# Kernel optimization log

Measured on AMD Instinct MI355X. Metric: run time of the kernel, lower is better.

The kernel has to match this reference:

```python
import jax, jax.numpy as jnp
import numpy as np

B, T, E, HD = 8, 2048, 1024, 64  # batch, seq (== n_ctx), n_embd, head_dim = n_embd // n_head


def setup_inputs() -> dict:
    key = jax.random.key(0)
    k1, k2, k3, k4 = jax.random.split(key, 4)
    x = jax.random.normal(k1, (B, T, E), dtype=jnp.float32)
    s = E ** -0.5  # Linear-like init scale
    Wq = jax.random.normal(k2, (E, HD), dtype=jnp.float32) * s
    Wk = jax.random.normal(k3, (E, HD), dtype=jnp.float32) * s
    Wv = jax.random.normal(k4, (E, HD), dtype=jnp.float32) * s
    return {"x": x, "Wq": Wq, "Wk": Wk, "Wv": Wv}


def reference(x, Wq, Wk, Wv):
    # q,k,v: [B, T, HD]
    q = jnp.einsum('bte,eh->bth', x, Wq)
    k = jnp.einsum('bte,eh->bth', x, Wk)
    v = jnp.einsum('bte,eh->bth', x, Wv)
    scale = k.shape[-1] ** -0.5
    # scores: [B, T, T]
    alpha = jnp.einsum('bqh,bkh->bqk', q, k) * scale
    causal = jnp.tril(jnp.ones((T, T), dtype=bool))
    alpha = jnp.where(causal, alpha, -jnp.inf)
    alpha = jax.nn.softmax(alpha, axis=-1)
    # dropout with p=0.0 is identity in eval
    h = jnp.einsum('bqk,bkh->bqh', alpha, v)  # [B, T, HD]
    return h
```

## Files before the change

### kernel.cpp

```cpp
#include <hip/hip_runtime.h>
#include <hip/hip_bf16.h>
#include <math.h>

#define BATCH 8
#define T 2048
#define E 1024
#define HD 64
#define BT (BATCH * T)

typedef __bf16 bf16_t;
typedef bf16_t bf16x4 __attribute__((ext_vector_type(4)));
typedef bf16_t bf16x8 __attribute__((ext_vector_type(8)));
typedef float f32x4 __attribute__((ext_vector_type(4)));

#define MFMA(a, b, c) __builtin_amdgcn_mfma_f32_16x16x32_bf16((a), (b), (c), 0, 0, 0)

#define QSCALE (0.125f * 1.44269504088896340736f)


__global__ __launch_bounds__(256) void prep_w(const float* __restrict__ Wq,
                                              const float* __restrict__ Wk,
                                              const float* __restrict__ Wv,
                                              bf16_t* __restrict__ WTt) {
    const int nt  = blockIdx.x >> 3;
    const int kc0 = (blockIdx.x & 7) * 128;
    const int tid = threadIdx.x;
    const int l16 = tid & 15;
    const int k8  = (kc0 >> 3) + (tid >> 4);
    const int n   = nt * 16 + l16;
    const int m   = n >> 6;
    const int col = n & 63;
    const float* W = (m == 0) ? Wq : (m == 1) ? Wk : Wv;
    const float scale = (m == 0) ? QSCALE : 1.0f;
    bf16x8 o;
#pragma unroll
    for (int j = 0; j < 8; j++) {
        o[j] = (bf16_t)(W[(size_t)(k8 * 8 + j) * HD + col] * scale);
    }
    *reinterpret_cast<bf16x8*>(WTt + (size_t)nt * 16384 + k8 * 128 + l16 * 8) = o;
}

__global__ __launch_bounds__(256) void qkv_proj(
    const float* __restrict__ x,
    const bf16_t* __restrict__ WTt,
    bf16_t* __restrict__ qt,
    bf16_t* __restrict__ kt,
    bf16_t* __restrict__ vt)
{
    const int cm   = blockIdx.x >> 8;
    const int rt   = blockIdx.x & 255;
    const int wave = threadIdx.x >> 6;
    const int lane = threadIdx.x & 63;
    const int l16  = lane & 15;
    const int quad = lane >> 4;
    const int rowbase = rt * 64 + wave * 16;

    const float*  arow  = x + (size_t)(rowbase + l16) * E + quad * 8;
    const bf16_t* bbase = WTt + (size_t)cm * 4 * 16384 + lane * 8;

    f32x4 acc[4] = {};

    f32x4 a0 = *reinterpret_cast<const f32x4*>(arow);
    f32x4 a1 = *reinterpret_cast<const f32x4*>(arow + 4);
    bf16x8 bf0 = *reinterpret_cast<const bf16x8*>(bbase);
    bf16x8 bf1 = *reinterpret_cast<const bf16x8*>(bbase + 16384);
    bf16x8 bf2 = *reinterpret_cast<const bf16x8*>(bbase + 32768);
    bf16x8 bf3 = *reinterpret_cast<const bf16x8*>(bbase + 49152);

    for (int kc = 0; kc < E; kc += 32) {
        const int kn = (kc + 32) & (E - 1);
        f32x4 na0 = *reinterpret_cast<const f32x4*>(arow + kn);
        f32x4 na1 = *reinterpret_cast<const f32x4*>(arow + kn + 4);
        bf16x8 nb0 = *reinterpret_cast<const bf16x8*>(bbase + kn * 16);
        bf16x8 nb1 = *reinterpret_cast<const bf16x8*>(bbase + kn * 16 + 16384);
        bf16x8 nb2 = *reinterpret_cast<const bf16x8*>(bbase + kn * 16 + 32768);
        bf16x8 nb3 = *reinterpret_cast<const bf16x8*>(bbase + kn * 16 + 49152);
        bf16x8 af;
#pragma unroll
        for (int j = 0; j < 4; j++) {
            af[j]     = (bf16_t)a0[j];
            af[4 + j] = (bf16_t)a1[j];
        }
        acc[0] = MFMA(af, bf0, acc[0]);
        acc[1] = MFMA(af, bf1, acc[1]);
        acc[2] = MFMA(af, bf2, acc[2]);
        acc[3] = MFMA(af, bf3, acc[3]);
        a0 = na0; a1 = na1;
        bf0 = nb0; bf1 = nb1; bf2 = nb2; bf3 = nb3;
    }

    if (cm < 2) {
        bf16_t* dst = (cm == 0) ? qt : kt;
        const size_t tbase = (size_t)(rowbase >> 4) * 1024;
#pragma unroll
        for (int tc = 0; tc < 4; tc++) {
            const size_t o0 = tbase + (size_t)(tc * 2 + (l16 >> 3)) * 128 + (l16 & 7);
#pragma unroll
            for (int r = 0; r < 4; r++) {
                dst[o0 + (quad * 4 + r) * 8] = (bf16_t)acc[tc][r];
            }
        }
    } else {
        const int b_    = rowbase >> 11;
        const int tbase = rowbase & (T - 1);
        const size_t o0 = (size_t)b_ * 131072 +
                          (size_t)((tbase >> 3) + (quad >> 1)) * 128 +
                          l16 * 8 + (quad & 1) * 4;
#pragma unroll
        for (int tc = 0; tc < 4; tc++) {
            bf16x4 pv;
#pragma unroll
            for (int r = 0; r < 4; r++) pv[r] = (bf16_t)acc[tc][r];
            *reinterpret_cast<bf16x4*>(vt + o0 + (size_t)tc * 32768) = pv;
        }
    }
}

__global__ __launch_bounds__(512) void attn(
    const bf16_t* __restrict__ qtl,
    const bf16_t* __restrict__ ktl,
    const bf16_t* __restrict__ vtl,
    float* __restrict__ out)
{
    __shared__ __align__(16) bf16_t plds[8][16][40];
    __shared__ float opart[8][16][66];
    __shared__ float lpart[8][16];

    const int wave = threadIdx.x >> 6;
    const int lane = threadIdx.x & 63;
    const int l16  = lane & 15;
    const int quad = lane >> 4;
    const int group = wave >> 2;
    const int kw    = wave & 3;

    const int b  = blockIdx.x >> 6;
    const int pr = blockIdx.x & 63;
    const int qt = group ? (127 - pr) : pr;
    const int rowbase = qt * 16;

    const bf16_t* Qb = qtl + (size_t)((b * T + rowbase) >> 4) * 1024 + lane * 8;
    const bf16_t* Kb = ktl + (size_t)b * T * 64 + lane * 8;
    const bf16_t* Vb = vtl + (size_t)b * 131072 + lane * 8;

    const bf16x8 qf0 = *reinterpret_cast<const bf16x8*>(Qb);
    const bf16x8 qf1 = *reinterpret_cast<const bf16x8*>(Qb + 512);

    f32x4 o[4] = {};
    f32x4 lrun = {};

    const int nch = (rowbase + 47) >> 5;

    int k0 = kw * 32;
    bf16x8 kfa0 = *reinterpret_cast<const bf16x8*>(Kb + k0 * 64);
    bf16x8 kfb0 = *reinterpret_cast<const bf16x8*>(Kb + k0 * 64 + 512);
    bf16x8 kfa1 = *reinterpret_cast<const bf16x8*>(Kb + k0 * 64 + 1024);
    bf16x8 kfb1 = *reinterpret_cast<const bf16x8*>(Kb + k0 * 64 + 1536);
    bf16x8 vf0 = *reinterpret_cast<const bf16x8*>(Vb + k0 * 16);
    bf16x8 vf1 = *reinterpret_cast<const bf16x8*>(Vb + k0 * 16 + 32768);
    bf16x8 vf2 = *reinterpret_cast<const bf16x8*>(Vb + k0 * 16 + 65536);
    bf16x8 vf3 = *reinterpret_cast<const bf16x8*>(Vb + k0 * 16 + 98304);

    for (int c = kw; c < nch; c += 4) {
        k0 = c * 32;
        const int cn = (c + 4 < nch) ? (c + 4) : c;
        const int kn = cn * 32;
        bf16x8 nkfa0 = *reinterpret_cast<const bf16x8*>(Kb + kn * 64);
        bf16x8 nkfb0 = *reinterpret_cast<const bf16x8*>(Kb + kn * 64 + 512);
        bf16x8 nkfa1 = *reinterpret_cast<const bf16x8*>(Kb + kn * 64 + 1024);
        bf16x8 nkfb1 = *reinterpret_cast<const bf16x8*>(Kb + kn * 64 + 1536);
        bf16x8 nvf0 = *reinterpret_cast<const bf16x8*>(Vb + kn * 16);
        bf16x8 nvf1 = *reinterpret_cast<const bf16x8*>(Vb + kn * 16 + 32768);
        bf16x8 nvf2 = *reinterpret_cast<const bf16x8*>(Vb + kn * 16 + 65536);
        bf16x8 nvf3 = *reinterpret_cast<const bf16x8*>(Vb + kn * 16 + 98304);

        f32x4 s_lo = {};
        f32x4 s_hi = {};
        s_lo = MFMA(qf0, kfa0, s_lo);
        s_lo = MFMA(qf1, kfb0, s_lo);
        s_hi = MFMA(qf0, kfa1, s_hi);
        s_hi = MFMA(qf1, kfb1, s_hi);

        if (k0 + 31 > rowbase) {
            const int row = rowbase + quad * 4;
#pragma unroll
            for (int r = 0; r < 4; r++) {
                if (k0 + l16 > row + r)      s_lo[r] = -INFINITY;
                if (k0 + 16 + l16 > row + r) s_hi[r] = -INFINITY;
            }
        }

#pragma unroll
        for (int r = 0; r < 4; r++) {
            const float p0 = exp2f(s_lo[r]);
            const float p1 = exp2f(s_hi[r]);
            lrun[r] += p0 + p1;
            plds[wave][quad * 4 + r][l16]      = (bf16_t)p0;
            plds[wave][quad * 4 + r][16 + l16] = (bf16_t)p1;
        }
        const bf16x8 pf = *reinterpret_cast<const bf16x8*>(&plds[wave][l16][quad * 8]);

        o[0] = MFMA(pf, vf0, o[0]);
        o[1] = MFMA(pf, vf1, o[1]);
        o[2] = MFMA(pf, vf2, o[2]);
        o[3] = MFMA(pf, vf3, o[3]);

        kfa0 = nkfa0; kfb0 = nkfb0; kfa1 = nkfa1; kfb1 = nkfb1;
        vf0 = nvf0; vf1 = nvf1; vf2 = nvf2; vf3 = nvf3;
    }

#pragma unroll
    for (int r = 0; r < 4; r++) {
        float l = lrun[r];
        l += __shfl_xor(l, 1);
        l += __shfl_xor(l, 2);
        l += __shfl_xor(l, 4);
        l += __shfl_xor(l, 8);
        if (l16 == 0) lpart[wave][quad * 4 + r] = l;
#pragma unroll
        for (int nb = 0; nb < 4; nb++) {
            opart[wave][quad * 4 + r][nb * 16 + l16] = o[nb][r];
        }
    }
    __syncthreads();

    const int g    = threadIdx.x >> 8;
    const int gtid = threadIdx.x & 255;
    const int qtg  = g ? (127 - pr) : pr;
    const size_t outbase = (size_t)b * T + qtg * 16;
#pragma unroll
    for (int pass = 0; pass < 4; pass++) {
        const int row = pass * 4 + (gtid >> 6);
        const int col = gtid & 63;
        float osum = 0.f, lsum = 0.f;
#pragma unroll
        for (int w = 0; w < 4; w++) {
            osum += opart[g * 4 + w][row][col];
            lsum += lpart[g * 4 + w][row];
        }
        out[(outbase + row) * HD + col] = osum / lsum;
    }
}

extern "C" void kernel_launch(void* const* d_in, const int* in_sizes, int n_in,
                              void* d_out, int out_size, void* d_ws, size_t ws_size,
                              hipStream_t stream) {
    const float* x  = (const float*)d_in[0];
    const float* Wq = (const float*)d_in[1];
    const float* Wk = (const float*)d_in[2];
    const float* Wv = (const float*)d_in[3];
    float* out = (float*)d_out;

    bf16_t* ws  = (bf16_t*)d_ws;
    bf16_t* WTt = ws;
    bf16_t* qtl = WTt + (size_t)192 * E;
    bf16_t* ktl = qtl + (size_t)BT * HD;
    bf16_t* vtl = ktl + (size_t)BT * HD;

    prep_w<<<96, 256, 0, stream>>>(Wq, Wk, Wv, WTt);
    qkv_proj<<<768, 256, 0, stream>>>(x, WTt, qtl, ktl, vtl);
    attn<<<512, 512, 0, stream>>>(qtl, ktl, vtl, out);
}
```

Baseline: 142.2 us.

## Split QKV column tiles and give each attention query tile its own block

qkv_proj now splits each 64-column output group into two halves across separate blocks, doubling the grid and halving per-block accumulators, with an occupancy hint. The attention kernel stops pairing two query tiles per block and assigns one query tile per block, with all 8 waves striding over key chunks. It drops register double-buffering of K/V and unions the P staging buffer with the reduction buffer to cut LDS use. The aim is more parallelism and occupancy. The cost is that the x rows are re-read twice in the projection, attention blocks are now imbalanced in length, and the K/V loads are no longer prefetched.

```diff
diff --git a/kernel.cpp b/kernel.cpp
--- a/kernel.cpp
+++ b/kernel.cpp
@@ -40,64 +40,66 @@
     *reinterpret_cast<bf16x8*>(WTt + (size_t)nt * 16384 + k8 * 128 + l16 * 8) = o;
 }
 
-__global__ __launch_bounds__(256) void qkv_proj(
+__global__ __launch_bounds__(256, 8) void qkv_proj(
     const float* __restrict__ x,
     const bf16_t* __restrict__ WTt,
     bf16_t* __restrict__ qt,
     bf16_t* __restrict__ kt,
     bf16_t* __restrict__ vt)
 {
-    const int cm   = blockIdx.x >> 8;
-    const int rt   = blockIdx.x & 255;
+    const int bx  = blockIdx.x;
+    const int cm  = bx / 512;
+    const int rem = bx - cm * 512;
+    const int rt  = rem >> 1;
+    const int ch  = rem & 1;
     const int wave = threadIdx.x >> 6;
     const int lane = threadIdx.x & 63;
     const int l16  = lane & 15;
     const int quad = lane >> 4;
     const int rowbase = rt * 64 + wave * 16;
 
-    const float*  arow  = x + (size_t)(rowbase + l16) * E + quad * 8;
-    const bf16_t* bbase = WTt + (size_t)cm * 4 * 16384 + lane * 8;
-
-    f32x4 acc[4] = {};
+    const float*  arow = x + (size_t)(rowbase + l16) * E + quad * 8;
+    const bf16_t* bb0  = WTt + (size_t)(cm * 4 + ch * 2) * 16384 + lane * 8;
+    const bf16_t* bb1  = bb0 + 16384;
+
+    f32x4 acc0 = {};
+    f32x4 acc1 = {};
 
     f32x4 a0 = *reinterpret_cast<const f32x4*>(arow);
     f32x4 a1 = *reinterpret_cast<const f32x4*>(arow + 4);
-    bf16x8 bf0 = *reinterpret_cast<const bf16x8*>(bbase);
-    bf16x8 bf1 = *reinterpret_cast<const bf16x8*>(bbase + 16384);
-    bf16x8 bf2 = *reinterpret_cast<const bf16x8*>(bbase + 32768);
-    bf16x8 bf3 = *reinterpret_cast<const bf16x8*>(bbase + 49152);
+    bf16x8 bf0 = *reinterpret_cast<const bf16x8*>(bb0);
+    bf16x8 bf1 = *reinterpret_cast<const bf16x8*>(bb1);
 
     for (int kc = 0; kc < E; kc += 32) {
         const int kn = (kc + 32) & (E - 1);
         f32x4 na0 = *reinterpret_cast<const f32x4*>(arow + kn);
         f32x4 na1 = *reinterpret_cast<const f32x4*>(arow + kn + 4);
-        bf16x8 nb0 = *reinterpret_cast<const bf16x8*>(bbase + kn * 16);
-        bf16x8 nb1 = *reinterpret_cast<const bf16x8*>(bbase + kn * 16 + 16384);
-        bf16x8 nb2 = *reinterpret_cast<const bf16x8*>(bbase + kn * 16 + 32768);
-        bf16x8 nb3 = *reinterpret_cast<const bf16x8*>(bbase + kn * 16 + 49152);
+        bf16x8 nb0 = *reinterpret_cast<const bf16x8*>(bb0 + kn * 16);
+        bf16x8 nb1 = *reinterpret_cast<const bf16x8*>(bb1 + kn * 16);
+
         bf16x8 af;
 #pragma unroll
         for (int j = 0; j < 4; j++) {
             af[j]     = (bf16_t)a0[j];
             af[4 + j] = (bf16_t)a1[j];
         }
-        acc[0] = MFMA(af, bf0, acc[0]);
-        acc[1] = MFMA(af, bf1, acc[1]);
-        acc[2] = MFMA(af, bf2, acc[2]);
-        acc[3] = MFMA(af, bf3, acc[3]);
-        a0 = na0; a1 = na1;
-        bf0 = nb0; bf1 = nb1; bf2 = nb2; bf3 = nb3;
+        acc0 = MFMA(af, bf0, acc0);
+        acc1 = MFMA(af, bf1, acc1);
+
+        a0 = na0; a1 = na1; bf0 = nb0; bf1 = nb1;
     }
 
     if (cm < 2) {
         bf16_t* dst = (cm == 0) ? qt : kt;
         const size_t tbase = (size_t)(rowbase >> 4) * 1024;
 #pragma unroll
-        for (int tc = 0; tc < 4; tc++) {
-            const size_t o0 = tbase + (size_t)(tc * 2 + (l16 >> 3)) * 128 + (l16 & 7);
+        for (int tc = 0; tc < 2; tc++) {
+            const int tcg = ch * 2 + tc;
+            const f32x4 acc = tc ? acc1 : acc0;
+            const size_t o0 = tbase + (size_t)(tcg * 2 + (l16 >> 3)) * 128 + (l16 & 7);
 #pragma unroll
             for (int r = 0; r < 4; r++) {
-                dst[o0 + (quad * 4 + r) * 8] = (bf16_t)acc[tc][r];
+                dst[o0 + (quad * 4 + r) * 8] = (bf16_t)acc[r];
             }
         }
     } else {
@@ -107,35 +109,37 @@
                           (size_t)((tbase >> 3) + (quad >> 1)) * 128 +
                           l16 * 8 + (quad & 1) * 4;
 #pragma unroll
-        for (int tc = 0; tc < 4; tc++) {
+        for (int tc = 0; tc < 2; tc++) {
+            const int tcg = ch * 2 + tc;
+            const f32x4 acc = tc ? acc1 : acc0;
             bf16x4 pv;
 #pragma unroll
-            for (int r = 0; r < 4; r++) pv[r] = (bf16_t)acc[tc][r];
-            *reinterpret_cast<bf16x4*>(vt + o0 + (size_t)tc * 32768) = pv;
-        }
-    }
-}
-
-__global__ __launch_bounds__(512) void attn(
+            for (int r = 0; r < 4; r++) pv[r] = (bf16_t)acc[r];
+            *reinterpret_cast<bf16x4*>(vt + o0 + (size_t)tcg * 32768) = pv;
+        }
+    }
+}
+
+__global__ __launch_bounds__(512, 6) void attn(
     const bf16_t* __restrict__ qtl,
     const bf16_t* __restrict__ ktl,
     const bf16_t* __restrict__ vtl,
     float* __restrict__ out)
 {
-    __shared__ __align__(16) bf16_t plds[8][16][40];
-    __shared__ float opart[8][16][66];
+    union SmemT {
+        float  opart[8][16][65];
+        bf16_t plds[8][16][40];
+    };
+    __shared__ __align__(16) SmemT sm;
     __shared__ float lpart[8][16];
 
     const int wave = threadIdx.x >> 6;
     const int lane = threadIdx.x & 63;
     const int l16  = lane & 15;
     const int quad = lane >> 4;
-    const int group = wave >> 2;
-    const int kw    = wave & 3;
-
-    const int b  = blockIdx.x >> 6;
-    const int pr = blockIdx.x & 63;
-    const int qt = group ? (127 - pr) : pr;
+
+    const int b  = blockIdx.x >> 7;
+    const int qt = 127 - (blockIdx.x & 127);
     const int rowbase = qt * 16;
 
     const bf16_t* Qb = qtl + (size_t)((b * T + rowbase) >> 4) * 1024 + lane * 8;
@@ -150,28 +154,19 @@
 
     const int nch = (rowbase + 47) >> 5;
 
-    int k0 = kw * 32;
-    bf16x8 kfa0 = *reinterpret_cast<const bf16x8*>(Kb + k0 * 64);
-    bf16x8 kfb0 = *reinterpret_cast<const bf16x8*>(Kb + k0 * 64 + 512);
-    bf16x8 kfa1 = *reinterpret_cast<const bf16x8*>(Kb + k0 * 64 + 1024);
-    bf16x8 kfb1 = *reinterpret_cast<const bf16x8*>(Kb + k0 * 64 + 1536);
-    bf16x8 vf0 = *reinterpret_cast<const bf16x8*>(Vb + k0 * 16);
-    bf16x8 vf1 = *reinterpret_cast<const bf16x8*>(Vb + k0 * 16 + 32768);
-    bf16x8 vf2 = *reinterpret_cast<const bf16x8*>(Vb + k0 * 16 + 65536);
-    bf16x8 vf3 = *reinterpret_cast<const bf16x8*>(Vb + k0 * 16 + 98304);
-
-    for (int c = kw; c < nch; c += 4) {
-        k0 = c * 32;
-        const int cn = (c + 4 < nch) ? (c + 4) : c;
-        const int kn = cn * 32;
-        bf16x8 nkfa0 = *reinterpret_cast<const bf16x8*>(Kb + kn * 64);
-        bf16x8 nkfb0 = *reinterpret_cast<const bf16x8*>(Kb + kn * 64 + 512);
-        bf16x8 nkfa1 = *reinterpret_cast<const bf16x8*>(Kb + kn * 64 + 1024);
-        bf16x8 nkfb1 = *reinterpret_cast<const bf16x8*>(Kb + kn * 64 + 1536);
-        bf16x8 nvf0 = *reinterpret_cast<const bf16x8*>(Vb + kn * 16);
-        bf16x8 nvf1 = *reinterpret_cast<const bf16x8*>(Vb + kn * 16 + 32768);
-        bf16x8 nvf2 = *reinterpret_cast<const bf16x8*>(Vb + kn * 16 + 65536);
-        bf16x8 nvf3 = *reinterpret_cast<const bf16x8*>(Vb + kn * 16 + 98304);
+    for (int c = wave; c < nch; c += 8) {
+        const int k0 = c * 32;
+
+        const bf16_t* kp = Kb + k0 * 64;
+        bf16x8 kfa0 = *reinterpret_cast<const bf16x8*>(kp);
+        bf16x8 kfb0 = *reinterpret_cast<const bf16x8*>(kp + 512);
+        bf16x8 kfa1 = *reinterpret_cast<const bf16x8*>(kp + 1024);
+        bf16x8 kfb1 = *reinterpret_cast<const bf16x8*>(kp + 1536);
+        const bf16_t* vp = Vb + k0 * 16;
+        bf16x8 vf0 = *reinterpret_cast<const bf16x8*>(vp);
+        bf16x8 vf1 = *reinterpret_cast<const bf16x8*>(vp + 32768);
+        bf16x8 vf2 = *reinterpret_cast<const bf16x8*>(vp + 65536);
+        bf16x8 vf3 = *reinterpret_cast<const bf16x8*>(vp + 98304);
 
         f32x4 s_lo = {};
         f32x4 s_hi = {};
@@ -194,19 +189,18 @@
             const float p0 = exp2f(s_lo[r]);
             const float p1 = exp2f(s_hi[r]);
             lrun[r] += p0 + p1;
-            plds[wave][quad * 4 + r][l16]      = (bf16_t)p0;
-            plds[wave][quad * 4 + r][16 + l16] = (bf16_t)p1;
-        }
-        const bf16x8 pf = *reinterpret_cast<const bf16x8*>(&plds[wave][l16][quad * 8]);
+            sm.plds[wave][quad * 4 + r][l16]      = (bf16_t)p0;
+            sm.plds[wave][quad * 4 + r][16 + l16] = (bf16_t)p1;
+        }
+        const bf16x8 pf = *reinterpret_cast<const bf16x8*>(&sm.plds[wave][l16][quad * 8]);
 
         o[0] = MFMA(pf, vf0, o[0]);
         o[1] = MFMA(pf, vf1, o[1]);
         o[2] = MFMA(pf, vf2, o[2]);
         o[3] = MFMA(pf, vf3, o[3]);
-
-        kfa0 = nkfa0; kfb0 = nkfb0; kfa1 = nkfa1; kfb1 = nkfb1;
-        vf0 = nvf0; vf1 = nvf1; vf2 = nvf2; vf3 = nvf3;
-    }
+    }
+
+    __syncthreads();
 
 #pragma unroll
     for (int r = 0; r < 4; r++) {
@@ -218,26 +212,22 @@
         if (l16 == 0) lpart[wave][quad * 4 + r] = l;
 #pragma unroll
         for (int nb = 0; nb < 4; nb++) {
-            opart[wave][quad * 4 + r][nb * 16 + l16] = o[nb][r];
+            sm.opart[wave][quad * 4 + r][nb * 16 + l16] = o[nb][r];
         }
     }
     __syncthreads();
 
-    const int g    = threadIdx.x >> 8;
-    const int gtid = threadIdx.x & 255;
-    const int qtg  = g ? (127 - pr) : pr;
-    const size_t outbase = (size_t)b * T + qtg * 16;
-#pragma unroll
-    for (int pass = 0; pass < 4; pass++) {
-        const int row = pass * 4 + (gtid >> 6);
-        const int col = gtid & 63;
+    const int col = threadIdx.x & 63;
+#pragma unroll
+    for (int pass = 0; pass < 2; pass++) {
+        const int row = pass * 8 + (threadIdx.x >> 6);
         float osum = 0.f, lsum = 0.f;
 #pragma unroll
-        for (int w = 0; w < 4; w++) {
-            osum += opart[g * 4 + w][row][col];
-            lsum += lpart[g * 4 + w][row];
-        }
-        out[(outbase + row) * HD + col] = osum / lsum;
+        for (int w = 0; w < 8; w++) {
+            osum += sm.opart[w][row][col];
+            lsum += lpart[w][row];
+        }
+        out[((size_t)b * T + rowbase + row) * HD + col] = osum / lsum;
     }
 }
 
@@ -257,6 +247,6 @@
     bf16_t* vtl = ktl + (size_t)BT * HD;
 
     prep_w<<<96, 256, 0, stream>>>(Wq, Wk, Wv, WTt);
-    qkv_proj<<<768, 256, 0, stream>>>(x, WTt, qtl, ktl, vtl);
-    attn<<<512, 512, 0, stream>>>(qtl, ktl, vtl, out);
-}
+    qkv_proj<<<1536, 256, 0, stream>>>(x, WTt, qtl, ktl, vtl);
+    attn<<<1024, 512, 0, stream>>>(qtl, ktl, vtl, out);
+}
```

Result: slower. 174.1 us (+22.4%).

## Compute all QKV columns per block so x is read once via LDS

Applied to the files above, without the earlier changes.

The QKV projection now has each block of 32 rows compute all 192 output columns, instead of splitting the columns across three blocks that each re-read x from global memory. x is loaded once per block, converted to bf16 and staged in a double-buffered LDS tile shared by the four waves, which are arranged as 2 row groups by 2 column halves of 6 MFMA tiles each. This is meant to cut redundant fp32 reads of x and conversion work, at the cost of a barrier per 64-wide k step, more accumulator registers, and fewer blocks (512 instead of 768).

```diff
diff --git a/kernel.cpp b/kernel.cpp
--- a/kernel.cpp
+++ b/kernel.cpp
@@ -40,78 +40,102 @@
     *reinterpret_cast<bf16x8*>(WTt + (size_t)nt * 16384 + k8 * 128 + l16 * 8) = o;
 }
 
-__global__ __launch_bounds__(256) void qkv_proj(
+__global__ __launch_bounds__(256, 4) void qkv_proj(
     const float* __restrict__ x,
     const bf16_t* __restrict__ WTt,
     bf16_t* __restrict__ qt,
     bf16_t* __restrict__ kt,
     bf16_t* __restrict__ vt)
 {
-    const int cm   = blockIdx.x >> 8;
-    const int rt   = blockIdx.x & 255;
-    const int wave = threadIdx.x >> 6;
-    const int lane = threadIdx.x & 63;
+    __shared__ __align__(16) bf16_t xbuf[2][32][72];
+
+    const int tid  = threadIdx.x;
+    const int wave = tid >> 6;
+    const int lane = tid & 63;
     const int l16  = lane & 15;
     const int quad = lane >> 4;
-    const int rowbase = rt * 64 + wave * 16;
-
-    const float*  arow  = x + (size_t)(rowbase + l16) * E + quad * 8;
-    const bf16_t* bbase = WTt + (size_t)cm * 4 * 16384 + lane * 8;
-
-    f32x4 acc[4] = {};
-
-    f32x4 a0 = *reinterpret_cast<const f32x4*>(arow);
-    f32x4 a1 = *reinterpret_cast<const f32x4*>(arow + 4);
-    bf16x8 bf0 = *reinterpret_cast<const bf16x8*>(bbase);
-    bf16x8 bf1 = *reinterpret_cast<const bf16x8*>(bbase + 16384);
-    bf16x8 bf2 = *reinterpret_cast<const bf16x8*>(bbase + 32768);
-    bf16x8 bf3 = *reinterpret_cast<const bf16x8*>(bbase + 49152);
-
-    for (int kc = 0; kc < E; kc += 32) {
-        const int kn = (kc + 32) & (E - 1);
-        f32x4 na0 = *reinterpret_cast<const f32x4*>(arow + kn);
-        f32x4 na1 = *reinterpret_cast<const f32x4*>(arow + kn + 4);
-        bf16x8 nb0 = *reinterpret_cast<const bf16x8*>(bbase + kn * 16);
-        bf16x8 nb1 = *reinterpret_cast<const bf16x8*>(bbase + kn * 16 + 16384);
-        bf16x8 nb2 = *reinterpret_cast<const bf16x8*>(bbase + kn * 16 + 32768);
-        bf16x8 nb3 = *reinterpret_cast<const bf16x8*>(bbase + kn * 16 + 49152);
-        bf16x8 af;
-#pragma unroll
-        for (int j = 0; j < 4; j++) {
-            af[j]     = (bf16_t)a0[j];
-            af[4 + j] = (bf16_t)a1[j];
-        }
-        acc[0] = MFMA(af, bf0, acc[0]);
-        acc[1] = MFMA(af, bf1, acc[1]);
-        acc[2] = MFMA(af, bf2, acc[2]);
-        acc[3] = MFMA(af, bf3, acc[3]);
-        a0 = na0; a1 = na1;
-        bf0 = nb0; bf1 = nb1; bf2 = nb2; bf3 = nb3;
-    }
-
-    if (cm < 2) {
-        bf16_t* dst = (cm == 0) ? qt : kt;
-        const size_t tbase = (size_t)(rowbase >> 4) * 1024;
-#pragma unroll
-        for (int tc = 0; tc < 4; tc++) {
-            const size_t o0 = tbase + (size_t)(tc * 2 + (l16 >> 3)) * 128 + (l16 & 7);
+    const int wr   = wave >> 1;
+    const int wc   = wave & 1;
+    const int rowbase0 = blockIdx.x * 32;
+
+    const int srow = tid >> 3;
+    const int sseg = tid & 7;
+    const float* xsrc = x + (size_t)(rowbase0 + srow) * E + sseg * 8;
+
+    f32x4 acc[6] = {};
+
+    {
+        f32x4 xa = *reinterpret_cast<const f32x4*>(xsrc);
+        f32x4 xb = *reinterpret_cast<const f32x4*>(xsrc + 4);
+        bf16x8 xw;
+#pragma unroll
+        for (int u = 0; u < 4; u++) {
+            xw[u]     = (bf16_t)xa[u];
+            xw[4 + u] = (bf16_t)xb[u];
+        }
+        *reinterpret_cast<bf16x8*>(&xbuf[0][srow][sseg * 8]) = xw;
+    }
+    __syncthreads();
+
+    int p = 0;
+    for (int kc = 0; kc < E; kc += 64) {
+        const int kn = (kc + 64) & (E - 1);
+        const f32x4 nxa = *reinterpret_cast<const f32x4*>(xsrc + kn);
+        const f32x4 nxb = *reinterpret_cast<const f32x4*>(xsrc + kn + 4);
+
+        bf16x8 bf[2][6];
+#pragma unroll
+        for (int ks = 0; ks < 2; ks++) {
+#pragma unroll
+            for (int tc = 0; tc < 6; tc++) {
+                bf[ks][tc] = *reinterpret_cast<const bf16x8*>(
+                    WTt + (size_t)(wc * 6 + tc) * 16384 + (kc + ks * 32) * 16 + lane * 8);
+            }
+        }
+
+        const bf16x8 a0 = *reinterpret_cast<const bf16x8*>(&xbuf[p][wr * 16 + l16][quad * 8]);
+        const bf16x8 a1 = *reinterpret_cast<const bf16x8*>(&xbuf[p][wr * 16 + l16][32 + quad * 8]);
+
+#pragma unroll
+        for (int tc = 0; tc < 6; tc++) acc[tc] = MFMA(a0, bf[0][tc], acc[tc]);
+#pragma unroll
+        for (int tc = 0; tc < 6; tc++) acc[tc] = MFMA(a1, bf[1][tc], acc[tc]);
+
+        bf16x8 xw;
+#pragma unroll
+        for (int u = 0; u < 4; u++) {
+            xw[u]     = (bf16_t)nxa[u];
+            xw[4 + u] = (bf16_t)nxb[u];
+        }
+        *reinterpret_cast<bf16x8*>(&xbuf[p ^ 1][srow][sseg * 8]) = xw;
+        __syncthreads();
+        p ^= 1;
+    }
+
+    const int rowbase = rowbase0 + wr * 16;
+#pragma unroll
+    for (int tc = 0; tc < 6; tc++) {
+        const int n0  = wc * 96 + tc * 16;
+        const int m   = n0 >> 6;
+        const int tcg = (n0 & 63) >> 4;
+        if (m < 2) {
+            bf16_t* dst = (m == 0) ? qt : kt;
+            const size_t o0 = (size_t)(rowbase >> 4) * 1024 +
+                              (size_t)(tcg * 2 + (l16 >> 3)) * 128 + (l16 & 7);
 #pragma unroll
             for (int r = 0; r < 4; r++) {
                 dst[o0 + (quad * 4 + r) * 8] = (bf16_t)acc[tc][r];
             }
-        }
-    } else {
-        const int b_    = rowbase >> 11;
-        const int tbase = rowbase & (T - 1);
-        const size_t o0 = (size_t)b_ * 131072 +
-                          (size_t)((tbase >> 3) + (quad >> 1)) * 128 +
-                          l16 * 8 + (quad & 1) * 4;
-#pragma unroll
-        for (int tc = 0; tc < 4; tc++) {
+        } else {
+            const int b_    = rowbase >> 11;
+            const int tbase = rowbase & (T - 1);
+            const size_t o0 = (size_t)b_ * 131072 +
+                              (size_t)((tbase >> 3) + (quad >> 1)) * 128 +
+                              l16 * 8 + (quad & 1) * 4 + (size_t)tcg * 32768;
             bf16x4 pv;
 #pragma unroll
             for (int r = 0; r < 4; r++) pv[r] = (bf16_t)acc[tc][r];
-            *reinterpret_cast<bf16x4*>(vt + o0 + (size_t)tc * 32768) = pv;
+            *reinterpret_cast<bf16x4*>(vt + o0) = pv;
         }
     }
 }
@@ -257,6 +281,6 @@
     bf16_t* vtl = ktl + (size_t)BT * HD;
 
     prep_w<<<96, 256, 0, stream>>>(Wq, Wk, Wv, WTt);
-    qkv_proj<<<768, 256, 0, stream>>>(x, WTt, qtl, ktl, vtl);
+    qkv_proj<<<512, 256, 0, stream>>>(x, WTt, qtl, ktl, vtl);
     attn<<<512, 512, 0, stream>>>(qtl, ktl, vtl, out);
 }
```

After: 132.3 us. 1.08x faster.
